# Performance work log

Measured on AMD Instinct MI355X. Metric: run time of the kernel, lower is better.

## Reference

```python
import jax, jax.numpy as jnp
import numpy as np

B, E, F1, F2, C = 8192, 8, 1024, 2048, 100


def setup_inputs() -> dict:
    key = jax.random.key(0)
    k = jax.random.split(key, 6)
    s1 = 1.0 / np.sqrt(F1)
    s2 = 1.0 / np.sqrt(F2)
    return {
        "domain": jax.random.randint(k[0], (B,), 0, E, dtype=jnp.int32),
        "x": jax.random.normal(k[1], (B, F1), dtype=jnp.float32),
        "W1": jax.random.normal(k[2], (E, F1, F2), dtype=jnp.float32) * s1,
        "b1": jax.random.normal(k[3], (E, F2), dtype=jnp.float32) * s1,
        "W2": jax.random.normal(k[4], (E, F2, C), dtype=jnp.float32) * s2,
        "b2": jax.random.normal(k[5], (E, C), dtype=jnp.float32) * s2,
    }


def reference(domain, x, W1, b1, W2, b2):
    # All-experts 2-layer MLP over the full batch (faithful to the torch loop,
    # expressed as batched einsums over the expert axis e).
    h = jax.nn.relu(jnp.einsum("bf,efh->beh", x, W1) + b1[None, :, :])  # [B,E,F2]
    logits = jnp.einsum("beh,ehc->bec", h, W2) + b2[None, :, :]          # [B,E,C]
    # Gather the expert selected by each sample's domain index.
    sel = jnp.take_along_axis(logits, domain[:, None, None].astype(jnp.int32), axis=1)
    sel = sel[:, 0, :]                                                    # [B,C]
    return jax.nn.softmax(sel, axis=-1)
```

## Files before the change

### kernel.cpp

```cpp
#include <hip/hip_runtime.h>
#include <math.h>

#define NB 8192
#define NE 8
#define F1 1024
#define F2 2048
#define NC 100
#define NCP 112
#define TM 128
#define BK 32
#define NKT (F1 / BK)
#define NCC (F2 / 128)
#define MAXTY 72

#define WS_CUR   17
#define WS_TYE   32
#define WS_TYR   104
#define WS_TYN   176
#define WS_ROWS  256

#define OFF_XH  ((size_t)65536)
#define SZ_X    ((size_t)NB * F1)
#define OFF_W1H (OFF_XH + 4 * SZ_X)
#define SZ_W1   ((size_t)NE * F2 * F1)
#define OFF_W2H (OFF_W1H + 4 * SZ_W1)
#define SZ_W2   ((size_t)NE * NCP * F2)

typedef float f32x4 __attribute__((ext_vector_type(4)));
typedef short s16x8 __attribute__((ext_vector_type(8)));
typedef unsigned short u16x8 __attribute__((ext_vector_type(8)));
typedef unsigned short u16x4 __attribute__((ext_vector_type(4)));

__device__ __forceinline__ unsigned short bf_hi(float f) {
    unsigned u = __float_as_uint(f);
    return (unsigned short)((u + 0x7FFFu + ((u >> 16) & 1u)) >> 16);
}
__device__ __forceinline__ float bf_up(unsigned short h) {
    return __uint_as_float(((unsigned)h) << 16);
}

typedef const __attribute__((address_space(1))) unsigned cgu;
typedef __attribute__((address_space(3))) unsigned ldu;
__device__ __forceinline__ void gl16(const void* g, void* l) {
    __builtin_amdgcn_global_load_lds((cgu*)g, (ldu*)l, 16, 0, 0);
}

__global__ __launch_bounds__(512) void k_plan(const int* __restrict__ dom, int* ws) {
    __shared__ int wh[8][8];
    const int tid = threadIdx.x, wave = tid >> 6, lane = tid & 63;
    int cnt[NE];
#pragma unroll
    for (int e = 0; e < NE; ++e) cnt[e] = 0;
    for (int i = tid; i < NB / 4; i += 512) {
        int4 d = ((const int4*)dom)[i];
        int v[4] = {d.x, d.y, d.z, d.w};
#pragma unroll
        for (int t = 0; t < 4; ++t)
#pragma unroll
            for (int e = 0; e < NE; ++e)
                cnt[e] += (int)__popcll(__ballot(v[t] == e));
    }
    if (lane == 0)
#pragma unroll
        for (int e = 0; e < NE; ++e) wh[wave][e] = cnt[e];
    __syncthreads();
    if (tid == 0) {
        int c[NE], off = 0, ty = 0;
        for (int e = 0; e < NE; ++e) {
            c[e] = 0;
            for (int w = 0; w < 8; ++w) c[e] += wh[w][e];
        }
        for (int e = 0; e < NE; ++e) {
            ws[WS_CUR + e] = off;
            int nt = (c[e] + TM - 1) / TM;
            for (int t = 0; t < nt; ++t) {
                ws[WS_TYE + ty] = e;
                ws[WS_TYR + ty] = off + t * TM;
                ws[WS_TYN + ty] = min(TM, c[e] - t * TM);
                ++ty;
            }
            off += c[e];
        }
        for (; ty < MAXTY; ++ty) ws[WS_TYN + ty] = 0;
    }
}

__global__ __launch_bounds__(256) void k_scatter(const int* __restrict__ dom, int* ws) {
    __shared__ int lh[NE], base[NE];
    const int tid = threadIdx.x;
    if (tid < NE) lh[tid] = 0;
    __syncthreads();
    const int b = blockIdx.x * 256 + tid;
    const int e = dom[b];
    const int r = atomicAdd(&lh[e], 1);
    __syncthreads();
    if (tid < NE) base[tid] = atomicAdd(&ws[WS_CUR + tid], lh[tid]);
    __syncthreads();
    ws[WS_ROWS + base[e] + r] = b;
}

__global__ __launch_bounds__(256) void k_prep(
    const float* __restrict__ x, const float* __restrict__ W1,
    const float* __restrict__ W2, unsigned short* __restrict__ xh,
    unsigned short* __restrict__ w1h, unsigned short* __restrict__ w2h)
{
    __shared__ float t[64 * 101];
    const int bx = blockIdx.x;
    if (bx < 2048) {
        unsigned short* xl = xh + SZ_X;
#pragma unroll
        for (int q = 0; q < 4; ++q) {
            size_t i = (size_t)bx * 1024 + q * 256 + threadIdx.x;
            float4 v = *(const float4*)(x + i * 4);
            u16x4 h, l;
            float f[4] = {v.x, v.y, v.z, v.w};
#pragma unroll
            for (int c = 0; c < 4; ++c) {
                unsigned short hh = bf_hi(f[c]);
                h[c] = hh;
                l[c] = bf_hi(f[c] - bf_up(hh));
            }
            *(u16x4*)(xh + i * 4) = h;
            *(u16x4*)(xl + i * 4) = l;
        }
    } else if (bx < 2048 + 4096) {
        unsigned short* w1l = w1h + SZ_W1;
        const int tt = bx - 2048;
        const int e = tt >> 9, rem = tt & 511;
        const int k0 = (rem >> 5) * 64, n0 = (rem & 31) * 64;
        const float* src = W1 + ((size_t)e * F1 + k0) * F2 + n0;
#pragma unroll
        for (int i = 0; i < 4; ++i) {
            int u = threadIdx.x + 256 * i;
            int k = u >> 4, n4 = (u & 15) * 4;
            float4 v = *(const float4*)(src + (size_t)k * F2 + n4);
            t[k * 65 + n4] = v.x; t[k * 65 + n4 + 1] = v.y;
            t[k * 65 + n4 + 2] = v.z; t[k * 65 + n4 + 3] = v.w;
        }
        __syncthreads();
#pragma unroll
        for (int i = 0; i < 2; ++i) {
            int u = threadIdx.x + 256 * i;
            int n = u >> 3, kg = u & 7;
            u16x8 hv, lv;
#pragma unroll
            for (int j = 0; j < 8; ++j) {
                float v = t[(kg * 8 + j) * 65 + n];
                unsigned short hh = bf_hi(v);
                hv[j] = hh;
                lv[j] = bf_hi(v - bf_up(hh));
            }
            size_t dst = ((size_t)e * F2 + n0 + n) * F1 + k0 + kg * 8;
            *(u16x8*)(w1h + dst) = hv;
            *(u16x8*)(w1l + dst) = lv;
        }
    } else {
        unsigned short* w2l = w2h + SZ_W2;
        const int tt = bx - 6144;
        const int e = tt >> 5, k0 = (tt & 31) * 64;
        const float* src = W2 + ((size_t)e * F2 + k0) * NC;
        for (int u = threadIdx.x; u < 64 * NC; u += 256) {
            int k = u / NC, c = u - k * NC;
            t[k * 101 + c] = src[u];
        }
        __syncthreads();
#pragma unroll
        for (int i = 0; i < 4; ++i) {
            int u = threadIdx.x + 256 * i;
            if (u < NCP * 8) {
                int c = u >> 3, kg = u & 7;
                u16x8 hv, lv;
#pragma unroll
                for (int j = 0; j < 8; ++j) {
                    float v = (c < NC) ? t[(kg * 8 + j) * 101 + c] : 0.f;
                    unsigned short hh = bf_hi(v);
                    hv[j] = hh;
                    lv[j] = bf_hi(v - bf_up(hh));
                }
                size_t dst = ((size_t)e * NCP + c) * F2 + k0 + kg * 8;
                *(u16x8*)(w2h + dst) = hv;
                *(u16x8*)(w2l + dst) = lv;
            }
        }
    }
}

__global__ __launch_bounds__(256, 2) void k_g1(
    const int* __restrict__ ws, const unsigned short* __restrict__ xh,
    const unsigned short* __restrict__ w1h, const unsigned short* __restrict__ w2h,
    const float* __restrict__ b1, float* __restrict__ out)
{
    __shared__ __align__(16) unsigned short sb[32768];
    __shared__ int rows[TM];
    const int tid = threadIdx.x;
    const int cc = blockIdx.x;
    const int ty = blockIdx.y;

    const int nr = ws[WS_TYN + ty];
    if (nr <= 0) return;
    const int e = ws[WS_TYE + ty];
    const int rbase = ws[WS_TYR + ty];
    if (tid < TM) rows[tid] = ws[WS_ROWS + rbase + min(tid, nr - 1)];
    __syncthreads();

    const int wave = tid >> 6, lane = tid & 63;
    const int wm = wave >> 1, wn = wave & 1;
    const int lg = lane >> 4, ln = lane & 15;
    const int l7 = ln & 7;

    const unsigned short* pA[2];
    const unsigned short* pB[2];
#pragma unroll
    for (int i = 0; i < 2; ++i) {
        int u = tid + 256 * i;
        int r = (u >> 6) * 16 + (u & 15), s = (u >> 4) & 3;
        pA[i] = xh + (size_t)rows[r] * F1 + s * 8;
        pB[i] = w1h + ((size_t)e * F2 + cc * 128 + r) * F1 + s * 8;
    }
    const int ldst0 = tid * 8;
    const int ldst1 = ldst0 + 2048;

    float bias[4];
#pragma unroll
    for (int nf = 0; nf < 4; ++nf)
        bias[nf] = b1[e * F2 + cc * 128 + wn * 64 + nf * 16 + ln];

    int aoff[4], boff[4];
#pragma unroll
    for (int m = 0; m < 4; ++m) aoff[m] = (wm * 4 + m) * 512 + lg * 128 + ln * 8;
#pragma unroll
    for (int n = 0; n < 4; ++n) boff[n] = 8192 + (wn * 4 + n) * 512 + lg * 128 + ln * 8;

    f32x4 acc[4][4];
#pragma unroll
    for (int m = 0; m < 4; ++m)
#pragma unroll
        for (int n = 0; n < 4; ++n) acc[m][n] = (f32x4){0.f, 0.f, 0.f, 0.f};

#define STAGE(kt, db)                                                          \
    {                                                                          \
        const int ko = (kt) * BK;                                              \
        const int b0 = (db) * 16384;                                           \
        gl16(pA[0] + ko,         &sb[b0 + ldst0]);                             \
        gl16(pA[1] + ko,         &sb[b0 + ldst1]);                             \
        gl16(pA[0] + SZ_X + ko,  &sb[b0 + 4096 + ldst0]);                      \
        gl16(pA[1] + SZ_X + ko,  &sb[b0 + 4096 + ldst1]);                      \
        gl16(pB[0] + ko,         &sb[b0 + 8192 + ldst0]);                      \
        gl16(pB[1] + ko,         &sb[b0 + 8192 + ldst1]);                      \
        gl16(pB[0] + SZ_W1 + ko, &sb[b0 + 12288 + ldst0]);                     \
        gl16(pB[1] + SZ_W1 + ko, &sb[b0 + 12288 + ldst1]);                     \
    }

    STAGE(0, 0);
    for (int kt = 0; kt < NKT; ++kt) {
        const int cur = kt & 1;
        if (kt + 1 < NKT) {
            STAGE(kt + 1, cur ^ 1);
            asm volatile("s_waitcnt vmcnt(8)" ::: "memory");
        } else {
            asm volatile("s_waitcnt vmcnt(0)" ::: "memory");
        }
        __builtin_amdgcn_s_barrier();
        __builtin_amdgcn_sched_barrier(0);
        const int b0 = cur * 16384;
        s16x8 ah[4], al[4];
#pragma unroll
        for (int m = 0; m < 4; ++m) {
            ah[m] = *(const s16x8*)&sb[b0 + aoff[m]];
            al[m] = *(const s16x8*)&sb[b0 + 4096 + aoff[m]];
        }
#pragma unroll
        for (int n = 0; n < 4; ++n) {
            s16x8 bh = *(const s16x8*)&sb[b0 + boff[n]];
            s16x8 bl = *(const s16x8*)&sb[b0 + 4096 + boff[n]];
#pragma unroll
            for (int m = 0; m < 4; ++m) {
                acc[m][n] = __builtin_amdgcn_mfma_f32_16x16x32_bf16(ah[m], bh, acc[m][n], 0, 0, 0);
                acc[m][n] = __builtin_amdgcn_mfma_f32_16x16x32_bf16(al[m], bh, acc[m][n], 0, 0, 0);
                acc[m][n] = __builtin_amdgcn_mfma_f32_16x16x32_bf16(ah[m], bl, acc[m][n], 0, 0, 0);
            }
        }
        __builtin_amdgcn_sched_barrier(0);
        __builtin_amdgcn_s_barrier();
    }
#undef STAGE

    f32x4 acc2[2][7];
#pragma unroll
    for (int mf = 0; mf < 2; ++mf)
#pragma unroll
        for (int cf = 0; cf < 7; ++cf) acc2[mf][cf] = (f32x4){0.f, 0.f, 0.f, 0.f};

#pragma unroll
    for (int s = 0; s < 2; ++s) {
        __syncthreads();
        if (wn == s) {
#pragma unroll
            for (int m = 0; m < 4; ++m)
#pragma unroll
                for (int nf = 0; nf < 4; ++nf) {
                    const float bb = bias[nf];
                    const int k2 = nf * 16 + ln;
#pragma unroll
                    for (int reg = 0; reg < 4; ++reg) {
                        int row = wm * 64 + m * 16 + lg * 4 + reg;
                        float v = fmaxf(acc[m][nf][reg] + bb, 0.f);
                        unsigned short hh = bf_hi(v);
                        int off = row * 64 + ((k2 >> 3) ^ (row & 7)) * 8 + (k2 & 7);
                        sb[off] = hh;
                        sb[8192 + off] = bf_hi(v - bf_up(hh));
                    }
                }
        }
        for (int ch = wave; ch < 14; ch += 4) {
            int u = ch * 64 + lane;
            int c = u >> 3, g = u & 7;
            const unsigned short* src =
                w2h + ((size_t)e * NCP + c) * F2 + cc * 128 + s * 64 + ((g ^ (c & 7)) * 8);
            gl16(src,         &sb[16384 + ch * 512]);
            gl16(src + SZ_W2, &sb[24576 + ch * 512]);
        }
        __syncthreads();
#pragma unroll
        for (int kk = 0; kk < 2; ++kk) {
            const int sz = (kk * 4 + lg) ^ l7;
            s16x8 hh[2], hl[2];
#pragma unroll
            for (int mf = 0; mf < 2; ++mf) {
                int off = (wave * 32 + mf * 16 + ln) * 64 + sz * 8;
                hh[mf] = *(const s16x8*)&sb[off];
                hl[mf] = *(const s16x8*)&sb[8192 + off];
            }
#pragma unroll
            for (int cf = 0; cf < 7; ++cf) {
                int off = (cf * 16 + ln) * 64 + sz * 8;
                s16x8 wh = *(const s16x8*)&sb[16384 + off];
                s16x8 wl = *(const s16x8*)&sb[24576 + off];
#pragma unroll
                for (int mf = 0; mf < 2; ++mf) {
                    acc2[mf][cf] = __builtin_amdgcn_mfma_f32_16x16x32_bf16(hh[mf], wh, acc2[mf][cf], 0, 0, 0);
                    acc2[mf][cf] = __builtin_amdgcn_mfma_f32_16x16x32_bf16(hl[mf], wh, acc2[mf][cf], 0, 0, 0);
                    acc2[mf][cf] = __builtin_amdgcn_mfma_f32_16x16x32_bf16(hh[mf], wl, acc2[mf][cf], 0, 0, 0);
                }
            }
        }
    }

#pragma unroll
    for (int mf = 0; mf < 2; ++mf)
#pragma unroll
        for (int cf = 0; cf < 7; ++cf)
#pragma unroll
            for (int reg = 0; reg < 4; ++reg) {
                int row = wave * 32 + mf * 16 + lg * 4 + reg;
                int c = cf * 16 + ln;
                if (row < nr && c < NC)
                    atomicAdd(out + (size_t)rows[row] * NC + c, acc2[mf][cf][reg]);
            }
}

__global__ void k_sm(const int* __restrict__ dom, const float* __restrict__ b2,
                     float* __restrict__ out)
{
    const int row = blockIdx.x * 4 + (threadIdx.x >> 6);
    const int lane = threadIdx.x & 63;
    const int e = dom[row];
    float* base = out + (size_t)row * NC;
    float v0 = base[lane] + b2[e * NC + lane];
    float v1 = -1e30f;
    if (lane + 64 < NC) v1 = base[lane + 64] + b2[e * NC + lane + 64];
    float m = fmaxf(v0, v1);
#pragma unroll
    for (int s = 1; s < 64; s <<= 1) m = fmaxf(m, __shfl_xor(m, s));
    float p0 = expf(v0 - m);
    float p1 = (lane + 64 < NC) ? expf(v1 - m) : 0.f;
    float sum = p0 + p1;
#pragma unroll
    for (int s = 1; s < 64; s <<= 1) sum += __shfl_xor(sum, s);
    float inv = 1.f / sum;
    base[lane] = p0 * inv;
    if (lane + 64 < NC) base[lane + 64] = p1 * inv;
}

extern "C" void kernel_launch(void* const* d_in, const int* in_sizes, int n_in,
                              void* d_out, int out_size, void* d_ws, size_t ws_size,
                              hipStream_t stream)
{
    const int*   dom = (const int*)d_in[0];
    const float* x   = (const float*)d_in[1];
    const float* W1  = (const float*)d_in[2];
    const float* b1  = (const float*)d_in[3];
    const float* W2  = (const float*)d_in[4];
    const float* b2  = (const float*)d_in[5];
    float*       out = (float*)d_out;
    int*         ws  = (int*)d_ws;

    unsigned short* xh  = (unsigned short*)((char*)d_ws + OFF_XH);
    unsigned short* w1h = (unsigned short*)((char*)d_ws + OFF_W1H);
    unsigned short* w2h = (unsigned short*)((char*)d_ws + OFF_W2H);

    hipMemsetAsync(out, 0, (size_t)NB * NC * sizeof(float), stream);
    hipLaunchKernelGGL(k_plan,    dim3(1), dim3(512), 0, stream, dom, ws);
    hipLaunchKernelGGL(k_scatter, dim3(NB / 256), dim3(256), 0, stream, dom, ws);
    hipLaunchKernelGGL(k_prep,    dim3(2048 + 4096 + 256), dim3(256), 0, stream,
                       x, W1, W2, xh, w1h, w2h);
    hipLaunchKernelGGL(k_g1,      dim3(NCC, MAXTY), dim3(256), 0, stream,
                       ws, xh, w1h, w2h, b1, out);
    hipLaunchKernelGGL(k_sm,      dim3(NB / 4), dim3(256), 0, stream, dom, b2, out);
}
```

Measured before the change: 412.4 us.

## Widen k_g1 column tile to 256 with 512 threads and single-buffered LDS

The fused first-layer/second-layer kernel now gives each block a 128x256 hidden-column tile with 8 waves (2x4) instead of 128x128 with 4 waves. This halves the number of column blocks, so gathered x rows are reloaded less often and fewer atomic partial sums reach the output. The explicit double-buffered staging with manual vmcnt waits is replaced by a single LDS buffer guarded by __syncthreads. The layer-2 stage is reorganised so each wave handles 16 rows over four 64-wide chunks. The trade-off is that global loads no longer overlap with MFMA work inside a block, and it relies on higher occupancy to hide that latency.

```diff
diff --git a/kernel.cpp b/kernel.cpp
--- a/kernel.cpp
+++ b/kernel.cpp
@@ -10,7 +10,8 @@
 #define TM 128
 #define BK 32
 #define NKT (F1 / BK)
-#define NCC (F2 / 128)
+#define CCW 256
+#define NCC (F2 / CCW)
 #define MAXTY 72
 
 #define WS_CUR   17
@@ -185,12 +186,12 @@
     }
 }
 
-__global__ __launch_bounds__(256, 2) void k_g1(
+__global__ __launch_bounds__(512, 4) void k_g1(
     const int* __restrict__ ws, const unsigned short* __restrict__ xh,
     const unsigned short* __restrict__ w1h, const unsigned short* __restrict__ w2h,
     const float* __restrict__ b1, float* __restrict__ out)
 {
-    __shared__ __align__(16) unsigned short sb[32768];
+    __shared__ __align__(16) unsigned short sb[30720];
     __shared__ int rows[TM];
     const int tid = threadIdx.x;
     const int cc = blockIdx.x;
@@ -204,32 +205,22 @@
     __syncthreads();
 
     const int wave = tid >> 6, lane = tid & 63;
-    const int wm = wave >> 1, wn = wave & 1;
+    const int wm = wave >> 2, wn = wave & 3;
     const int lg = lane >> 4, ln = lane & 15;
     const int l7 = ln & 7;
 
-    const unsigned short* pA[2];
-    const unsigned short* pB[2];
-#pragma unroll
-    for (int i = 0; i < 2; ++i) {
-        int u = tid + 256 * i;
-        int r = (u >> 6) * 16 + (u & 15), s = (u >> 4) & 3;
-        pA[i] = xh + (size_t)rows[r] * F1 + s * 8;
-        pB[i] = w1h + ((size_t)e * F2 + cc * 128 + r) * F1 + s * 8;
-    }
-    const int ldst0 = tid * 8;
-    const int ldst1 = ldst0 + 2048;
+    const int rA = tid >> 2, sA = tid & 3;
+    const unsigned short* pA  = xh + (size_t)rows[rA] * F1 + sA * 8;
+    const unsigned short* pB0 = w1h + ((size_t)e * F2 + cc * CCW + rA) * F1 + sA * 8;
+    const unsigned short* pB1 = pB0 + (size_t)128 * F1;
 
     float bias[4];
 #pragma unroll
     for (int nf = 0; nf < 4; ++nf)
-        bias[nf] = b1[e * F2 + cc * 128 + wn * 64 + nf * 16 + ln];
-
-    int aoff[4], boff[4];
-#pragma unroll
-    for (int m = 0; m < 4; ++m) aoff[m] = (wm * 4 + m) * 512 + lg * 128 + ln * 8;
-#pragma unroll
-    for (int n = 0; n < 4; ++n) boff[n] = 8192 + (wn * 4 + n) * 512 + lg * 128 + ln * 8;
+        bias[nf] = b1[e * F2 + cc * CCW + wn * 64 + nf * 16 + ln];
+
+    const int aoff0 = ((wm * 64 + ln) * 4 + lg) * 8;
+    const int boff0 = 8192 + ((wn * 64 + ln) * 4 + lg) * 8;
 
     f32x4 acc[4][4];
 #pragma unroll
@@ -237,42 +228,25 @@
 #pragma unroll
         for (int n = 0; n < 4; ++n) acc[m][n] = (f32x4){0.f, 0.f, 0.f, 0.f};
 
-#define STAGE(kt, db)                                                          \
-    {                                                                          \
-        const int ko = (kt) * BK;                                              \
-        const int b0 = (db) * 16384;                                           \
-        gl16(pA[0] + ko,         &sb[b0 + ldst0]);                             \
-        gl16(pA[1] + ko,         &sb[b0 + ldst1]);                             \
-        gl16(pA[0] + SZ_X + ko,  &sb[b0 + 4096 + ldst0]);                      \
-        gl16(pA[1] + SZ_X + ko,  &sb[b0 + 4096 + ldst1]);                      \
-        gl16(pB[0] + ko,         &sb[b0 + 8192 + ldst0]);                      \
-        gl16(pB[1] + ko,         &sb[b0 + 8192 + ldst1]);                      \
-        gl16(pB[0] + SZ_W1 + ko, &sb[b0 + 12288 + ldst0]);                     \
-        gl16(pB[1] + SZ_W1 + ko, &sb[b0 + 12288 + ldst1]);                     \
-    }
-
-    STAGE(0, 0);
     for (int kt = 0; kt < NKT; ++kt) {
-        const int cur = kt & 1;
-        if (kt + 1 < NKT) {
-            STAGE(kt + 1, cur ^ 1);
-            asm volatile("s_waitcnt vmcnt(8)" ::: "memory");
-        } else {
-            asm volatile("s_waitcnt vmcnt(0)" ::: "memory");
-        }
-        __builtin_amdgcn_s_barrier();
-        __builtin_amdgcn_sched_barrier(0);
-        const int b0 = cur * 16384;
+        const int ko = kt * BK;
+        gl16(pA + ko,          &sb[tid * 8]);
+        gl16(pA + SZ_X + ko,   &sb[4096 + tid * 8]);
+        gl16(pB0 + ko,         &sb[8192 + tid * 8]);
+        gl16(pB1 + ko,         &sb[12288 + tid * 8]);
+        gl16(pB0 + SZ_W1 + ko, &sb[16384 + tid * 8]);
+        gl16(pB1 + SZ_W1 + ko, &sb[20480 + tid * 8]);
+        __syncthreads();
         s16x8 ah[4], al[4];
 #pragma unroll
         for (int m = 0; m < 4; ++m) {
-            ah[m] = *(const s16x8*)&sb[b0 + aoff[m]];
-            al[m] = *(const s16x8*)&sb[b0 + 4096 + aoff[m]];
+            ah[m] = *(const s16x8*)&sb[aoff0 + m * 512];
+            al[m] = *(const s16x8*)&sb[4096 + aoff0 + m * 512];
         }
 #pragma unroll
         for (int n = 0; n < 4; ++n) {
-            s16x8 bh = *(const s16x8*)&sb[b0 + boff[n]];
-            s16x8 bl = *(const s16x8*)&sb[b0 + 4096 + boff[n]];
+            s16x8 bh = *(const s16x8*)&sb[boff0 + n * 512];
+            s16x8 bl = *(const s16x8*)&sb[8192 + boff0 + n * 512];
 #pragma unroll
             for (int m = 0; m < 4; ++m) {
                 acc[m][n] = __builtin_amdgcn_mfma_f32_16x16x32_bf16(ah[m], bh, acc[m][n], 0, 0, 0);
@@ -280,19 +254,14 @@
                 acc[m][n] = __builtin_amdgcn_mfma_f32_16x16x32_bf16(ah[m], bl, acc[m][n], 0, 0, 0);
             }
         }
-        __builtin_amdgcn_sched_barrier(0);
-        __builtin_amdgcn_s_barrier();
-    }
-#undef STAGE
-
-    f32x4 acc2[2][7];
-#pragma unroll
-    for (int mf = 0; mf < 2; ++mf)
-#pragma unroll
-        for (int cf = 0; cf < 7; ++cf) acc2[mf][cf] = (f32x4){0.f, 0.f, 0.f, 0.f};
-
-#pragma unroll
-    for (int s = 0; s < 2; ++s) {
+        __syncthreads();
+    }
+
+    f32x4 acc2[7];
+#pragma unroll
+    for (int cf = 0; cf < 7; ++cf) acc2[cf] = (f32x4){0.f, 0.f, 0.f, 0.f};
+
+    for (int s = 0; s < 4; ++s) {
         __syncthreads();
         if (wn == s) {
 #pragma unroll
@@ -312,51 +281,44 @@
                     }
                 }
         }
-        for (int ch = wave; ch < 14; ch += 4) {
-            int u = ch * 64 + lane;
+        for (int u = tid; u < 896; u += 512) {
             int c = u >> 3, g = u & 7;
             const unsigned short* src =
-                w2h + ((size_t)e * NCP + c) * F2 + cc * 128 + s * 64 + ((g ^ (c & 7)) * 8);
-            gl16(src,         &sb[16384 + ch * 512]);
-            gl16(src + SZ_W2, &sb[24576 + ch * 512]);
+                w2h + ((size_t)e * NCP + c) * F2 + cc * CCW + s * 64 + ((g ^ (c & 7)) * 8);
+            gl16(src,         &sb[16384 + u * 8]);
+            gl16(src + SZ_W2, &sb[23552 + u * 8]);
         }
         __syncthreads();
 #pragma unroll
         for (int kk = 0; kk < 2; ++kk) {
             const int sz = (kk * 4 + lg) ^ l7;
-            s16x8 hh[2], hl[2];
-#pragma unroll
-            for (int mf = 0; mf < 2; ++mf) {
-                int off = (wave * 32 + mf * 16 + ln) * 64 + sz * 8;
-                hh[mf] = *(const s16x8*)&sb[off];
-                hl[mf] = *(const s16x8*)&sb[8192 + off];
-            }
+            const int hoff = (wave * 16 + ln) * 64 + sz * 8;
+            s16x8 hhv = *(const s16x8*)&sb[hoff];
+            s16x8 hlv = *(const s16x8*)&sb[8192 + hoff];
 #pragma unroll
             for (int cf = 0; cf < 7; ++cf) {
-                int off = (cf * 16 + ln) * 64 + sz * 8;
-                s16x8 wh = *(const s16x8*)&sb[16384 + off];
-                s16x8 wl = *(const s16x8*)&sb[24576 + off];
-#pragma unroll
-                for (int mf = 0; mf < 2; ++mf) {
-                    acc2[mf][cf] = __builtin_amdgcn_mfma_f32_16x16x32_bf16(hh[mf], wh, acc2[mf][cf], 0, 0, 0);
-                    acc2[mf][cf] = __builtin_amdgcn_mfma_f32_16x16x32_bf16(hl[mf], wh, acc2[mf][cf], 0, 0, 0);
-                    acc2[mf][cf] = __builtin_amdgcn_mfma_f32_16x16x32_bf16(hh[mf], wl, acc2[mf][cf], 0, 0, 0);
-                }
-            }
-        }
-    }
-
-#pragma unroll
-    for (int mf = 0; mf < 2; ++mf)
-#pragma unroll
-        for (int cf = 0; cf < 7; ++cf)
-#pragma unroll
-            for (int reg = 0; reg < 4; ++reg) {
-                int row = wave * 32 + mf * 16 + lg * 4 + reg;
-                int c = cf * 16 + ln;
-                if (row < nr && c < NC)
-                    atomicAdd(out + (size_t)rows[row] * NC + c, acc2[mf][cf][reg]);
-            }
+                const int woff = 16384 + (cf * 16 + ln) * 64 + sz * 8;
+                s16x8 wh = *(const s16x8*)&sb[woff];
+                s16x8 wl = *(const s16x8*)&sb[woff + 7168];
+                acc2[cf] = __builtin_amdgcn_mfma_f32_16x16x32_bf16(hhv, wh, acc2[cf], 0, 0, 0);
+                acc2[cf] = __builtin_amdgcn_mfma_f32_16x16x32_bf16(hlv, wh, acc2[cf], 0, 0, 0);
+                acc2[cf] = __builtin_amdgcn_mfma_f32_16x16x32_bf16(hhv, wl, acc2[cf], 0, 0, 0);
+            }
+        }
+    }
+
+#pragma unroll
+    for (int cf = 0; cf < 7; ++cf) {
+        int c = cf * 16 + ln;
+        if (c < NC) {
+#pragma unroll
+            for (int i = 0; i < 4; ++i) {
+                int row = wave * 16 + lg * 4 + i;
+                if (row < nr)
+                    atomicAdd(out + (size_t)rows[row] * NC + c, acc2[cf][i]);
+            }
+        }
+    }
 }
 
 __global__ void k_sm(const int* __restrict__ dom, const float* __restrict__ b2,
@@ -404,7 +366,7 @@
     hipLaunchKernelGGL(k_scatter, dim3(NB / 256), dim3(256), 0, stream, dom, ws);
     hipLaunchKernelGGL(k_prep,    dim3(2048 + 4096 + 256), dim3(256), 0, stream,
                        x, W1, W2, xh, w1h, w2h);
-    hipLaunchKernelGGL(k_g1,      dim3(NCC, MAXTY), dim3(256), 0, stream,
+    hipLaunchKernelGGL(k_g1,      dim3(NCC, MAXTY), dim3(512), 0, stream,
                        ws, xh, w1h, w2h, b1, out);
     hipLaunchKernelGGL(k_sm,      dim3(NB / 4), dim3(256), 0, stream, dom, b2, out);
 }
```

Result: slower. 558.5 us (+35.4%).

## Halve LDS to single buffer, raise occupancy, restage second GEMM in K=32 slices

Applied to the files above, without the earlier changes.

Cuts the k_g1 shared-memory tile from 64KB to 32KB by dropping the double-buffered global-to-LDS pipeline in favour of a single buffer with syncthreads around each K step, and raises launch bounds from 2 to 4 blocks per CU. The fused second GEMM is restaged in four K=32 slices without the XOR swizzle so it fits in the smaller buffer. The intent is to hide latency through more resident blocks rather than intra-block prefetch. The risks are exposed load latency per iteration, possible LDS bank conflicts without the swizzle, and register pressure under the tighter launch bound.

```diff
diff --git a/kernel.cpp b/kernel.cpp
--- a/kernel.cpp
+++ b/kernel.cpp
@@ -185,12 +185,12 @@
     }
 }
 
-__global__ __launch_bounds__(256, 2) void k_g1(
+__global__ __launch_bounds__(256, 4) void k_g1(
     const int* __restrict__ ws, const unsigned short* __restrict__ xh,
     const unsigned short* __restrict__ w1h, const unsigned short* __restrict__ w2h,
     const float* __restrict__ b1, float* __restrict__ out)
 {
-    __shared__ __align__(16) unsigned short sb[32768];
+    __shared__ __align__(16) unsigned short sb[16384];
     __shared__ int rows[TM];
     const int tid = threadIdx.x;
     const int cc = blockIdx.x;
@@ -206,19 +206,17 @@
     const int wave = tid >> 6, lane = tid & 63;
     const int wm = wave >> 1, wn = wave & 1;
     const int lg = lane >> 4, ln = lane & 15;
-    const int l7 = ln & 7;
 
     const unsigned short* pA[2];
     const unsigned short* pB[2];
 #pragma unroll
     for (int i = 0; i < 2; ++i) {
         int u = tid + 256 * i;
-        int r = (u >> 6) * 16 + (u & 15), s = (u >> 4) & 3;
+        int r = ((u >> 6) << 4) + (u & 15), s = (u >> 4) & 3;
         pA[i] = xh + (size_t)rows[r] * F1 + s * 8;
         pB[i] = w1h + ((size_t)e * F2 + cc * 128 + r) * F1 + s * 8;
     }
-    const int ldst0 = tid * 8;
-    const int ldst1 = ldst0 + 2048;
+    const int ldst0 = tid * 8, ldst1 = ldst0 + 2048;
 
     float bias[4];
 #pragma unroll
@@ -227,9 +225,9 @@
 
     int aoff[4], boff[4];
 #pragma unroll
-    for (int m = 0; m < 4; ++m) aoff[m] = (wm * 4 + m) * 512 + lg * 128 + ln * 8;
-#pragma unroll
-    for (int n = 0; n < 4; ++n) boff[n] = 8192 + (wn * 4 + n) * 512 + lg * 128 + ln * 8;
+    for (int m = 0; m < 4; ++m) aoff[m] = ((wm * 4 + m) * 64 + lg * 16 + ln) * 8;
+#pragma unroll
+    for (int n = 0; n < 4; ++n) boff[n] = 8192 + ((wn * 4 + n) * 64 + lg * 16 + ln) * 8;
 
     f32x4 acc[4][4];
 #pragma unroll
@@ -237,42 +235,27 @@
 #pragma unroll
         for (int n = 0; n < 4; ++n) acc[m][n] = (f32x4){0.f, 0.f, 0.f, 0.f};
 
-#define STAGE(kt, db)                                                          \
-    {                                                                          \
-        const int ko = (kt) * BK;                                              \
-        const int b0 = (db) * 16384;                                           \
-        gl16(pA[0] + ko,         &sb[b0 + ldst0]);                             \
-        gl16(pA[1] + ko,         &sb[b0 + ldst1]);                             \
-        gl16(pA[0] + SZ_X + ko,  &sb[b0 + 4096 + ldst0]);                      \
-        gl16(pA[1] + SZ_X + ko,  &sb[b0 + 4096 + ldst1]);                      \
-        gl16(pB[0] + ko,         &sb[b0 + 8192 + ldst0]);                      \
-        gl16(pB[1] + ko,         &sb[b0 + 8192 + ldst1]);                      \
-        gl16(pB[0] + SZ_W1 + ko, &sb[b0 + 12288 + ldst0]);                     \
-        gl16(pB[1] + SZ_W1 + ko, &sb[b0 + 12288 + ldst1]);                     \
-    }
-
-    STAGE(0, 0);
     for (int kt = 0; kt < NKT; ++kt) {
-        const int cur = kt & 1;
-        if (kt + 1 < NKT) {
-            STAGE(kt + 1, cur ^ 1);
-            asm volatile("s_waitcnt vmcnt(8)" ::: "memory");
-        } else {
-            asm volatile("s_waitcnt vmcnt(0)" ::: "memory");
-        }
-        __builtin_amdgcn_s_barrier();
-        __builtin_amdgcn_sched_barrier(0);
-        const int b0 = cur * 16384;
+        const int ko = kt * BK;
+        gl16(pA[0] + ko,          &sb[ldst0]);
+        gl16(pA[1] + ko,          &sb[ldst1]);
+        gl16(pA[0] + SZ_X + ko,   &sb[4096 + ldst0]);
+        gl16(pA[1] + SZ_X + ko,   &sb[4096 + ldst1]);
+        gl16(pB[0] + ko,          &sb[8192 + ldst0]);
+        gl16(pB[1] + ko,          &sb[8192 + ldst1]);
+        gl16(pB[0] + SZ_W1 + ko,  &sb[12288 + ldst0]);
+        gl16(pB[1] + SZ_W1 + ko,  &sb[12288 + ldst1]);
+        __syncthreads();
         s16x8 ah[4], al[4];
 #pragma unroll
         for (int m = 0; m < 4; ++m) {
-            ah[m] = *(const s16x8*)&sb[b0 + aoff[m]];
-            al[m] = *(const s16x8*)&sb[b0 + 4096 + aoff[m]];
+            ah[m] = *(const s16x8*)&sb[aoff[m]];
+            al[m] = *(const s16x8*)&sb[4096 + aoff[m]];
         }
 #pragma unroll
         for (int n = 0; n < 4; ++n) {
-            s16x8 bh = *(const s16x8*)&sb[b0 + boff[n]];
-            s16x8 bl = *(const s16x8*)&sb[b0 + 4096 + boff[n]];
+            s16x8 bh = *(const s16x8*)&sb[boff[n]];
+            s16x8 bl = *(const s16x8*)&sb[4096 + boff[n]];
 #pragma unroll
             for (int m = 0; m < 4; ++m) {
                 acc[m][n] = __builtin_amdgcn_mfma_f32_16x16x32_bf16(ah[m], bh, acc[m][n], 0, 0, 0);
@@ -280,10 +263,8 @@
                 acc[m][n] = __builtin_amdgcn_mfma_f32_16x16x32_bf16(ah[m], bl, acc[m][n], 0, 0, 0);
             }
         }
-        __builtin_amdgcn_sched_barrier(0);
-        __builtin_amdgcn_s_barrier();
-    }
-#undef STAGE
+        __syncthreads();
+    }
 
     f32x4 acc2[2][7];
 #pragma unroll
@@ -291,72 +272,79 @@
 #pragma unroll
         for (int cf = 0; cf < 7; ++cf) acc2[mf][cf] = (f32x4){0.f, 0.f, 0.f, 0.f};
 
-#pragma unroll
-    for (int s = 0; s < 2; ++s) {
-        __syncthreads();
-        if (wn == s) {
+    for (int sl = 0; sl < 4; ++sl) {
+        if (wn == (sl >> 1)) {
 #pragma unroll
             for (int m = 0; m < 4; ++m)
 #pragma unroll
-                for (int nf = 0; nf < 4; ++nf) {
+                for (int nfh = 0; nfh < 2; ++nfh) {
+                    const int nf = (sl & 1) * 2 + nfh;
                     const float bb = bias[nf];
-                    const int k2 = nf * 16 + ln;
+                    const int k2 = nfh * 16 + ln;
+                    const int su = (k2 >> 3) * 16;
 #pragma unroll
                     for (int reg = 0; reg < 4; ++reg) {
-                        int row = wm * 64 + m * 16 + lg * 4 + reg;
+                        const int r = wm * 64 + m * 16 + lg * 4 + reg;
                         float v = fmaxf(acc[m][nf][reg] + bb, 0.f);
                         unsigned short hh = bf_hi(v);
-                        int off = row * 64 + ((k2 >> 3) ^ (row & 7)) * 8 + (k2 & 7);
+                        int off = (((r >> 4) << 6) + su + (r & 15)) * 8 + (k2 & 7);
                         sb[off] = hh;
-                        sb[8192 + off] = bf_hi(v - bf_up(hh));
+                        sb[4096 + off] = bf_hi(v - bf_up(hh));
                     }
                 }
         }
-        for (int ch = wave; ch < 14; ch += 4) {
-            int u = ch * 64 + lane;
-            int c = u >> 3, g = u & 7;
+        {
+            int u = tid;
+            int c = ((u >> 6) << 4) + (u & 15), s = (u >> 4) & 3;
             const unsigned short* src =
-                w2h + ((size_t)e * NCP + c) * F2 + cc * 128 + s * 64 + ((g ^ (c & 7)) * 8);
-            gl16(src,         &sb[16384 + ch * 512]);
-            gl16(src + SZ_W2, &sb[24576 + ch * 512]);
-        }
-        __syncthreads();
-#pragma unroll
-        for (int kk = 0; kk < 2; ++kk) {
-            const int sz = (kk * 4 + lg) ^ l7;
-            s16x8 hh[2], hl[2];
+                w2h + ((size_t)e * NCP + c) * F2 + cc * 128 + sl * 32 + s * 8;
+            gl16(src,         &sb[8192 + u * 8]);
+            gl16(src + SZ_W2, &sb[11776 + u * 8]);
+            if (tid < 192) {
+                u = tid + 256;
+                c = ((u >> 6) << 4) + (u & 15); s = (u >> 4) & 3;
+                src = w2h + ((size_t)e * NCP + c) * F2 + cc * 128 + sl * 32 + s * 8;
+                gl16(src,         &sb[8192 + u * 8]);
+                gl16(src + SZ_W2, &sb[11776 + u * 8]);
+            }
+        }
+        __syncthreads();
+        s16x8 hh[2], hl[2];
+#pragma unroll
+        for (int mf = 0; mf < 2; ++mf) {
+            int off = ((wave * 2 + mf) * 64 + lg * 16 + ln) * 8;
+            hh[mf] = *(const s16x8*)&sb[off];
+            hl[mf] = *(const s16x8*)&sb[4096 + off];
+        }
+#pragma unroll
+        for (int cf = 0; cf < 7; ++cf) {
+            int off = 8192 + (cf * 64 + lg * 16 + ln) * 8;
+            s16x8 wh = *(const s16x8*)&sb[off];
+            s16x8 wl = *(const s16x8*)&sb[3584 + off];
 #pragma unroll
             for (int mf = 0; mf < 2; ++mf) {
-                int off = (wave * 32 + mf * 16 + ln) * 64 + sz * 8;
-                hh[mf] = *(const s16x8*)&sb[off];
-                hl[mf] = *(const s16x8*)&sb[8192 + off];
-            }
-#pragma unroll
-            for (int cf = 0; cf < 7; ++cf) {
-                int off = (cf * 16 + ln) * 64 + sz * 8;
-                s16x8 wh = *(const s16x8*)&sb[16384 + off];
-                s16x8 wl = *(const s16x8*)&sb[24576 + off];
-#pragma unroll
-                for (int mf = 0; mf < 2; ++mf) {
-                    acc2[mf][cf] = __builtin_amdgcn_mfma_f32_16x16x32_bf16(hh[mf], wh, acc2[mf][cf], 0, 0, 0);
-                    acc2[mf][cf] = __builtin_amdgcn_mfma_f32_16x16x32_bf16(hl[mf], wh, acc2[mf][cf], 0, 0, 0);
-                    acc2[mf][cf] = __builtin_amdgcn_mfma_f32_16x16x32_bf16(hh[mf], wl, acc2[mf][cf], 0, 0, 0);
+                acc2[mf][cf] = __builtin_amdgcn_mfma_f32_16x16x32_bf16(hh[mf], wh, acc2[mf][cf], 0, 0, 0);
+                acc2[mf][cf] = __builtin_amdgcn_mfma_f32_16x16x32_bf16(hl[mf], wh, acc2[mf][cf], 0, 0, 0);
+                acc2[mf][cf] = __builtin_amdgcn_mfma_f32_16x16x32_bf16(hh[mf], wl, acc2[mf][cf], 0, 0, 0);
+            }
+        }
+        __syncthreads();
+    }
+
+#pragma unroll
+    for (int mf = 0; mf < 2; ++mf)
+#pragma unroll
+        for (int cf = 0; cf < 7; ++cf) {
+            int c = cf * 16 + ln;
+            if (c < NC) {
+#pragma unroll
+                for (int reg = 0; reg < 4; ++reg) {
+                    int row = wave * 32 + mf * 16 + lg * 4 + reg;
+                    if (row < nr)
+                        atomicAdd(out + (size_t)rows[row] * NC + c, acc2[mf][cf][reg]);
                 }
             }
         }
-    }
-
-#pragma unroll
-    for (int mf = 0; mf < 2; ++mf)
-#pragma unroll
-        for (int cf = 0; cf < 7; ++cf)
-#pragma unroll
-            for (int reg = 0; reg < 4; ++reg) {
-                int row = wave * 32 + mf * 16 + lg * 4 + reg;
-                int c = cf * 16 + ln;
-                if (row < nr && c < NC)
-                    atomicAdd(out + (size_t)rows[row] * NC + c, acc2[mf][cf][reg]);
-            }
 }
 
 __global__ void k_sm(const int* __restrict__ dom, const float* __restrict__ b2,
```

Result: slower. 718.1 us (+74.1%).
